# Performance work log

Measured on AMD Instinct MI355X. Metric: run time of the kernel, lower is better.

The kernel has to match this reference:

```python
import jax, jax.numpy as jnp
import numpy as np

EPS = 1e-7
TOTAL_COUNT = 10000.0
BN_EPS = 1e-5
LEAKY_SLOPE = 0.2


def _gcn(h, src, dst, n):
    # GCNConv with add_self_loops=True, bias=False; h = x @ W already applied.
    # deg counts incoming edges at dst plus the self-loop weight of 1.
    deg = jax.ops.segment_sum(jnp.ones(src.shape[0], h.dtype), dst, num_segments=n) + 1.0
    dinv = jax.lax.rsqrt(deg)
    norm = dinv[src] * dinv[dst]                       # [E]
    agg = jax.ops.segment_sum(h[src] * norm[:, None], dst, num_segments=n)
    # self-loop contribution: norm_ii = dinv_i^2
    return agg + (dinv * dinv)[:, None] * h


def _bn(h, gamma, beta):
    # BatchNorm1d, training-mode batch statistics (biased variance)
    mu = h.mean(axis=0)
    var = h.var(axis=0)
    return gamma * (h - mu) * jax.lax.rsqrt(var + BN_EPS) + beta


def _layer(h, W, gamma, beta, src, dst, n):
    h = _gcn(h @ W, src, dst, n)
    h = _bn(h, gamma, beta)
    # LeakyReLU(0.2); Dropout treated as eval-mode identity
    return jnp.where(h >= 0, h, LEAKY_SLOPE * h)


def setup_inputs() -> dict:
    key = jax.random.key(0)
    ks = jax.random.split(key, 8)
    N, E, F_in, H, F_out = 50000, 800000, 1000, 256, 32
    return {
        "x": jax.random.uniform(ks[0], (N, F_in), jnp.float32),
        "W1": jax.random.normal(ks[1], (F_in, H), jnp.float32) * 0.05,
        "gamma1": jnp.ones((H,), jnp.float32),
        "beta1": jnp.zeros((H,), jnp.float32),
        "W2": jax.random.normal(ks[2], (H, H), jnp.float32) * 0.05,
        "gamma2": jnp.ones((H,), jnp.float32),
        "beta2": jnp.zeros((H,), jnp.float32),
        "W_loc": jax.random.normal(ks[3], (H, F_out), jnp.float32) * 0.05,
        "b_loc": jnp.zeros((F_out,), jnp.float32),
        "W_std": jax.random.normal(ks[4], (H, F_out), jnp.float32) * 0.05,
        "b_std": jnp.zeros((F_out,), jnp.float32),
        "edge_index": jax.random.randint(ks[5], (2, E), 0, N),
    }


def reference(x, W1, gamma1, beta1, W2, gamma2, beta2, W_loc, b_loc, W_std, b_std, edge_index):
    n = x.shape[0]
    src, dst = edge_index[0], edge_index[1]
    # normalize='log': library size then log1p of CPM-style scaling
    l = x.sum(axis=1, keepdims=True)                   # [N,1]
    h = jnp.log1p(x * (TOTAL_COUNT / l))
    h = _layer(h, W1, gamma1, beta1, src, dst, n)
    h = _layer(h, W2, gamma2, beta2, src, dst, n)
    loc = h @ W_loc + b_loc
    std = jax.nn.softplus(h @ W_std + b_std) + EPS     # Normal(loc, std) params
    return loc, std, l
```

## Files before the change

kernel.cpp:

```cpp
#include <hip/hip_runtime.h>
#include <hip/hip_bf16.h>


typedef float f32x4 __attribute__((ext_vector_type(4)));
typedef __bf16 bf16x8 __attribute__((ext_vector_type(8)));

#define AS1 __attribute__((address_space(1)))
#define AS3 __attribute__((address_space(3)))

__device__ __forceinline__ void gload_lds16(const void* g, void* l) {
  __builtin_amdgcn_global_load_lds((AS1 void*)(g), (AS3 void*)(l), 16, 0, 0);
}

__device__ __forceinline__ unsigned short f2bu(float f) {
  return __builtin_bit_cast(unsigned short, __float2bfloat16(f));
}
__device__ __forceinline__ float b2f(unsigned short u) {
  return __uint_as_float(((unsigned)u) << 16);
}

__device__ __forceinline__ void unpack8(uint4 v, float* f) {
  f[0] = __uint_as_float(v.x << 16);
  f[1] = __uint_as_float(v.x & 0xffff0000u);
  f[2] = __uint_as_float(v.y << 16);
  f[3] = __uint_as_float(v.y & 0xffff0000u);
  f[4] = __uint_as_float(v.z << 16);
  f[5] = __uint_as_float(v.z & 0xffff0000u);
  f[6] = __uint_as_float(v.w << 16);
  f[7] = __uint_as_float(v.w & 0xffff0000u);
}

__global__ void zero_k(int* __restrict__ p, int n) {
  int i = blockIdx.x * 256 + threadIdx.x;
  if (i < n) p[i] = 0;
}

__global__ void prep_w(const float* __restrict__ W1, const float* __restrict__ W2,
                       const float* __restrict__ Wloc, const float* __restrict__ Wstd,
                       unsigned short* __restrict__ W1T, unsigned short* __restrict__ W2T,
                       unsigned short* __restrict__ WcT) {
  int id = blockIdx.x * 256 + threadIdx.x;
  if (id < 262144) {
    int n = id >> 10, k = id & 1023;
    W1T[n * 1024 + k] = (k < 1000) ? f2bu(W1[k * 256 + n]) : (unsigned short)0;
  } else if (id < 262144 + 65536) {
    int id2 = id - 262144;
    int n = id2 >> 8, k = id2 & 255;
    W2T[n * 256 + k] = f2bu(W2[k * 256 + n]);
  } else if (id < 262144 + 65536 + 16384) {
    int id3 = id - 262144 - 65536;
    int j = id3 >> 8, k = id3 & 255;
    float v = (j < 32) ? Wloc[k * 32 + j] : Wstd[k * 32 + (j - 32)];
    WcT[j * 256 + k] = f2bu(v);
  }
}

__global__ __launch_bounds__(256) void rowsum_k(const float* __restrict__ X,
                                                float* __restrict__ out_l,
                                                unsigned short* __restrict__ xb, int n) {
  int gtid = blockIdx.x * 256 + threadIdx.x;
  int wave = gtid >> 6, lane = gtid & 63;
  int nw = (gridDim.x * 256) >> 6;
  for (int r = wave; r < n; r += nw) {
    const float4* xr = (const float4*)(X + (size_t)r * 1000);
    float4 v0 = xr[lane];
    float4 v1 = xr[lane + 64];
    float4 v2 = xr[lane + 128];
    float4 v3 = (lane < 58) ? xr[lane + 192] : make_float4(0.f, 0.f, 0.f, 0.f);
    float s = ((v0.x + v0.y) + (v0.z + v0.w)) + ((v1.x + v1.y) + (v1.z + v1.w)) +
              ((v2.x + v2.y) + (v2.z + v2.w)) + ((v3.x + v3.y) + (v3.z + v3.w));
#pragma unroll
    for (int o2 = 32; o2 > 0; o2 >>= 1) s += __shfl_xor(s, o2, 64);
    if (lane == 0) out_l[r] = s;
    float sc = 10000.f / s;
    unsigned short* xrow = xb + (size_t)r * 1024;
    ushort4 b;
    b.x = f2bu(__logf(fmaf(v0.x, sc, 1.f)));
    b.y = f2bu(__logf(fmaf(v0.y, sc, 1.f)));
    b.z = f2bu(__logf(fmaf(v0.z, sc, 1.f)));
    b.w = f2bu(__logf(fmaf(v0.w, sc, 1.f)));
    *(ushort4*)(xrow + lane * 4) = b;
    b.x = f2bu(__logf(fmaf(v1.x, sc, 1.f)));
    b.y = f2bu(__logf(fmaf(v1.y, sc, 1.f)));
    b.z = f2bu(__logf(fmaf(v1.z, sc, 1.f)));
    b.w = f2bu(__logf(fmaf(v1.w, sc, 1.f)));
    *(ushort4*)(xrow + (lane + 64) * 4) = b;
    b.x = f2bu(__logf(fmaf(v2.x, sc, 1.f)));
    b.y = f2bu(__logf(fmaf(v2.y, sc, 1.f)));
    b.z = f2bu(__logf(fmaf(v2.z, sc, 1.f)));
    b.w = f2bu(__logf(fmaf(v2.w, sc, 1.f)));
    *(ushort4*)(xrow + (lane + 128) * 4) = b;
    b.x = f2bu(__logf(fmaf(v3.x, sc, 1.f)));
    b.y = f2bu(__logf(fmaf(v3.y, sc, 1.f)));
    b.z = f2bu(__logf(fmaf(v3.z, sc, 1.f)));
    b.w = f2bu(__logf(fmaf(v3.w, sc, 1.f)));
    *(ushort4*)(xrow + (lane + 192) * 4) = b;
  }
}

__global__ void deg_k(const int* __restrict__ ei, int E, int* __restrict__ deg) {
  int e = blockIdx.x * blockDim.x + threadIdx.x;
  int stride = gridDim.x * blockDim.x;
  for (; e < E; e += stride) atomicAdd(&deg[ei[E + e]], 1);
}

__global__ __launch_bounds__(256) void scan1_k(const int* __restrict__ deg, int n,
                                               int* __restrict__ bsum,
                                               float* __restrict__ dinv) {
  int i = blockIdx.x * 256 + threadIdx.x;
  int v = (i < n) ? deg[i] : 0;
  if (i < n) dinv[i] = rsqrtf((float)v + 1.0f);
  __shared__ int sh[256];
  sh[threadIdx.x] = v;
  __syncthreads();
  for (int off = 128; off > 0; off >>= 1) {
    if (threadIdx.x < off) sh[threadIdx.x] += sh[threadIdx.x + off];
    __syncthreads();
  }
  if (threadIdx.x == 0) bsum[blockIdx.x] = sh[0];
}

__global__ __launch_bounds__(256) void scan2_k(int* __restrict__ bsum, int nb) {
  int t = threadIdx.x;
  int v = (t < nb) ? bsum[t] : 0;
  __shared__ int sh[256];
  sh[t] = v;
  __syncthreads();
  for (int off = 1; off < 256; off <<= 1) {
    int u = 0;
    if (t >= off) u = sh[t - off];
    __syncthreads();
    sh[t] += u;
    __syncthreads();
  }
  if (t < nb) bsum[t] = sh[t] - v;
}

__global__ __launch_bounds__(256) void scan3_k(const int* __restrict__ deg, int n, int E,
                                               const int* __restrict__ bsum,
                                               int* __restrict__ row_start,
                                               int* __restrict__ cursor) {
  int i = blockIdx.x * 256 + threadIdx.x;
  int t = threadIdx.x;
  int v = (i < n) ? deg[i] : 0;
  __shared__ int sh[256];
  sh[t] = v;
  __syncthreads();
  for (int off = 1; off < 256; off <<= 1) {
    int u = 0;
    if (t >= off) u = sh[t - off];
    __syncthreads();
    sh[t] += u;
    __syncthreads();
  }
  if (i < n) {
    int rs = bsum[blockIdx.x] + sh[t] - v;
    row_start[i] = rs;
    cursor[i] = rs;
    if (i == n - 1) row_start[n] = E;
  }
}

__global__ void scatter_k(const int* __restrict__ ei, int E,
                          const float* __restrict__ dinv, int* __restrict__ cursor,
                          int2* __restrict__ ew) {
  int e = blockIdx.x * blockDim.x + threadIdx.x;
  int stride = gridDim.x * blockDim.x;
  for (; e < E; e += stride) {
    int s = ei[e], d = ei[E + e];
    float w = dinv[s] * dinv[d];
    int pos = atomicAdd(&cursor[d], 1);
    ew[pos] = make_int2(s, __float_as_int(w));
  }
}

__global__ __launch_bounds__(256) void agg_k(const unsigned short* __restrict__ hg,
                                             const float* __restrict__ dinv,
                                             const int* __restrict__ row_start,
                                             const int2* __restrict__ ew,
                                             unsigned short* __restrict__ hout,
                                             float* __restrict__ psum,
                                             float* __restrict__ psum2, int n) {
  const int tid = threadIdx.x, lane = tid & 63, wid = tid >> 6;
  const int half = lane >> 5;
  const int fl = (lane & 31) * 8;
  int gwave = blockIdx.x * 4 + wid;
  int nw = gridDim.x * 4;
  float bs0 = 0.f, bs1 = 0.f, bs2 = 0.f, bs3 = 0.f;
  float bq0 = 0.f, bq1 = 0.f, bq2 = 0.f, bq3 = 0.f;
  for (int i = gwave; i < n; i += nw) {
    float di = dinv[i];
    float acc[8], f[8];
    {
      uint4 v = *(const uint4*)(hg + (size_t)i * 256 + fl);
      float w0 = half ? 0.f : di * di;
      unpack8(v, f);
#pragma unroll
      for (int q = 0; q < 8; ++q) acc[q] = w0 * f[q];
    }
    int e0 = row_start[i], e1 = row_start[i + 1];
    int j = e0;
    for (; j + 4 <= e1; j += 4) {
      int2 eA = ew[j + half];
      int2 eB = ew[j + 2 + half];
      float wA = __int_as_float(eA.y);
      float wB = __int_as_float(eB.y);
      uint4 vA = *(const uint4*)(hg + (size_t)eA.x * 256 + fl);
      uint4 vB = *(const uint4*)(hg + (size_t)eB.x * 256 + fl);
      float fa[8], fb[8];
      unpack8(vA, fa);
      unpack8(vB, fb);
#pragma unroll
      for (int q = 0; q < 8; ++q) acc[q] = fmaf(wA, fa[q], acc[q]);
#pragma unroll
      for (int q = 0; q < 8; ++q) acc[q] = fmaf(wB, fb[q], acc[q]);
    }
    if (j + 2 <= e1) {
      int2 eA = ew[j + half];
      float wA = __int_as_float(eA.y);
      uint4 vA = *(const uint4*)(hg + (size_t)eA.x * 256 + fl);
      unpack8(vA, f);
#pragma unroll
      for (int q = 0; q < 8; ++q) acc[q] = fmaf(wA, f[q], acc[q]);
      j += 2;
    }
    if (j < e1 && !half) {
      int2 eA = ew[j];
      float wA = __int_as_float(eA.y);
      uint4 vA = *(const uint4*)(hg + (size_t)eA.x * 256 + fl);
      unpack8(vA, f);
#pragma unroll
      for (int q = 0; q < 8; ++q) acc[q] = fmaf(wA, f[q], acc[q]);
    }
#pragma unroll
    for (int q = 0; q < 8; ++q) acc[q] += __shfl_xor(acc[q], 32, 64);
    float o0 = half ? acc[4] : acc[0];
    float o1 = half ? acc[5] : acc[1];
    float o2 = half ? acc[6] : acc[2];
    float o3 = half ? acc[7] : acc[3];
    ushort4 ob;
    ob.x = f2bu(o0); ob.y = f2bu(o1); ob.z = f2bu(o2); ob.w = f2bu(o3);
    *(ushort4*)(hout + (size_t)i * 256 + fl + half * 4) = ob;
    bs0 += o0; bq0 = fmaf(o0, o0, bq0);
    bs1 += o1; bq1 = fmaf(o1, o1, bq1);
    bs2 += o2; bq2 = fmaf(o2, o2, bq2);
    bs3 += o3; bq3 = fmaf(o3, o3, bq3);
  }
  __shared__ float ls[2048];
  int fbase = fl + half * 4;
  *(float4*)&ls[wid * 256 + fbase] = (float4){bs0, bs1, bs2, bs3};
  *(float4*)&ls[1024 + wid * 256 + fbase] = (float4){bq0, bq1, bq2, bq3};
  __syncthreads();
  float ss = ls[tid] + ls[256 + tid] + ls[512 + tid] + ls[768 + tid];
  float qq = ls[1024 + tid] + ls[1280 + tid] + ls[1536 + tid] + ls[1792 + tid];
  psum[(size_t)blockIdx.x * 256 + tid] = ss;
  psum2[(size_t)blockIdx.x * 256 + tid] = qq;
}

__global__ __launch_bounds__(256) void bnfinal_k(const float* __restrict__ psum,
                                                 const float* __restrict__ psum2,
                                                 int nb, int n,
                                                 const float* __restrict__ gamma,
                                                 const float* __restrict__ beta,
                                                 float* __restrict__ bnA,
                                                 float* __restrict__ bnB) {
  int f = blockIdx.x;
  int t = threadIdx.x;
  float s = 0.f, s2 = 0.f;
  for (int b = t; b < nb; b += 256) {
    s += psum[(size_t)b * 256 + f];
    s2 += psum2[(size_t)b * 256 + f];
  }
  __shared__ float as[256], as2[256];
  as[t] = s; as2[t] = s2;
  __syncthreads();
  for (int off = 128; off > 0; off >>= 1) {
    if (t < off) { as[t] += as[t + off]; as2[t] += as2[t + off]; }
    __syncthreads();
  }
  if (t == 0) {
    float m = as[0] / n;
    float var = as2[0] / n - m * m;
    float a = gamma[f] * rsqrtf(var + 1e-5f);
    bnA[f] = a;
    bnB[f] = beta[f] - m * a;
  }
}

template <int KSTEPS, int MODE>
__global__ __launch_bounds__(512) void gemm_kernel(
    const unsigned short* __restrict__ Abf, const unsigned short* __restrict__ Hb,
    const float* __restrict__ bnA, const float* __restrict__ bnB,
    const unsigned short* __restrict__ BT,
    unsigned short* __restrict__ C, int nrows) {
  __shared__ __align__(16) unsigned short At[128 * 64];
  __shared__ __align__(16) unsigned short Bt[256 * 64];
  const int tid = threadIdx.x;
  const int lane = tid & 63;
  const int wid = tid >> 6;
  const int wm = wid >> 2, wn = wid & 3;
  const int brow = blockIdx.x * 128;
  constexpr int K = KSTEPS * 64;

  f32x4 acc[4][4];
#pragma unroll
  for (int m = 0; m < 4; ++m)
#pragma unroll
    for (int n = 0; n < 4; ++n) acc[m][n] = (f32x4){0.f, 0.f, 0.f, 0.f};

  const int rloc = tid >> 4;
  const int hc = tid & 15;
  int growA[4];
#pragma unroll
  for (int p = 0; p < 4; ++p) {
    int r = p * 32 + rloc;
    int g = brow + r;
    if (g > nrows - 1) g = nrows - 1;
    growA[p] = g;
  }

  for (int ks = 0; ks < KSTEPS; ++ks) {
    const int k0 = ks * 64;
#pragma unroll
    for (int is = 0; is < 4; ++is) {
      int n0 = is * 64 + wid * 8;
      int nr = n0 + (lane >> 3);
      int csw = (lane & 7) ^ (lane >> 3);
      gload_lds16(BT + (size_t)nr * K + k0 + csw * 8, Bt + n0 * 64);
    }
    if constexpr (MODE == 0) {
#pragma unroll
      for (int is = 0; is < 2; ++is) {
        int r0 = is * 64 + wid * 8;
        int r = r0 + (lane >> 3);
        int g = brow + r;
        if (g > nrows - 1) g = nrows - 1;
        int csw = (lane & 7) ^ (lane >> 3);
        gload_lds16(Abf + (size_t)g * K + k0 + csw * 8, At + r0 * 64);
      }
    } else {
#pragma unroll
      for (int p = 0; p < 4; ++p) {
        int r = p * 32 + rloc;
        int kk = k0 + hc * 4;
        ushort4 v = *(const ushort4*)(Hb + (size_t)growA[p] * 256 + kk);
        float4 a = *(const float4*)(bnA + kk);
        float4 bb = *(const float4*)(bnB + kk);
        float y0 = fmaf(b2f(v.x), a.x, bb.x); y0 = y0 >= 0.f ? y0 : 0.2f * y0;
        float y1 = fmaf(b2f(v.y), a.y, bb.y); y1 = y1 >= 0.f ? y1 : 0.2f * y1;
        float y2 = fmaf(b2f(v.z), a.z, bb.z); y2 = y2 >= 0.f ? y2 : 0.2f * y2;
        float y3 = fmaf(b2f(v.w), a.w, bb.w); y3 = y3 >= 0.f ? y3 : 0.2f * y3;
        ushort4 b;
        b.x = f2bu(y0); b.y = f2bu(y1); b.z = f2bu(y2); b.w = f2bu(y3);
        *(ushort4*)((char*)At + r * 128 + ((hc * 8) ^ ((r & 7) << 4))) = b;
      }
    }
    __syncthreads();
#pragma unroll
    for (int kk2 = 0; kk2 < 2; ++kk2) {
      const int kb = kk2 * 64 + ((lane >> 4) << 4);
      bf16x8 afr[4], bfr[4];
#pragma unroll
      for (int m = 0; m < 4; ++m) {
        int row = wm * 64 + m * 16 + (lane & 15);
        afr[m] = *(const bf16x8*)((const char*)At + row * 128 + (kb ^ ((row & 7) << 4)));
      }
#pragma unroll
      for (int n = 0; n < 4; ++n) {
        int col = wn * 64 + n * 16 + (lane & 15);
        bfr[n] = *(const bf16x8*)((const char*)Bt + col * 128 + (kb ^ ((col & 7) << 4)));
      }
#pragma unroll
      for (int m = 0; m < 4; ++m)
#pragma unroll
        for (int n = 0; n < 4; ++n)
          acc[m][n] = __builtin_amdgcn_mfma_f32_16x16x32_bf16(afr[m], bfr[n], acc[m][n], 0, 0, 0);
    }
    __syncthreads();
  }
  const int cl = lane & 15;
  const int r4 = (lane >> 4) * 4;
#pragma unroll
  for (int m = 0; m < 4; ++m) {
    int row0 = brow + wm * 64 + m * 16 + r4;
#pragma unroll
    for (int n = 0; n < 4; ++n) {
      int col = wn * 64 + n * 16 + cl;
#pragma unroll
      for (int q = 0; q < 4; ++q) {
        int row = row0 + q;
        if (row < nrows) C[(size_t)row * 256 + col] = f2bu(acc[m][n][q]);
      }
    }
  }
}

__global__ __launch_bounds__(256) void head_kernel(
    const unsigned short* __restrict__ Hb, const float* __restrict__ bnA,
    const float* __restrict__ bnB, const unsigned short* __restrict__ BT,
    const float* __restrict__ bloc, const float* __restrict__ bstd,
    float* __restrict__ out, int nrows) {
  __shared__ __align__(16) unsigned short At[128 * 64];
  __shared__ __align__(16) unsigned short Bt[64 * 64];
  const int tid = threadIdx.x, lane = tid & 63, wid = tid >> 6;
  const int wm = wid >> 1, wn = wid & 1;
  const int brow = blockIdx.x * 128;

  f32x4 acc[4][2];
#pragma unroll
  for (int m = 0; m < 4; ++m)
#pragma unroll
    for (int n = 0; n < 2; ++n) acc[m][n] = (f32x4){0.f, 0.f, 0.f, 0.f};

  const int hc = tid & 15;
  for (int ks = 0; ks < 4; ++ks) {
    const int k0 = ks * 64;
#pragma unroll
    for (int is = 0; is < 2; ++is) {
      int n0 = is * 32 + wid * 8;
      int nr = n0 + (lane >> 3);
      int csw = (lane & 7) ^ (lane >> 3);
      gload_lds16(BT + (size_t)nr * 256 + k0 + csw * 8, Bt + n0 * 64);
    }
#pragma unroll
    for (int p = 0; p < 8; ++p) {
      int r = p * 16 + (tid >> 4);
      int g = brow + r;
      if (g > nrows - 1) g = nrows - 1;
      int kk = k0 + hc * 4;
      ushort4 v = *(const ushort4*)(Hb + (size_t)g * 256 + kk);
      float4 a = *(const float4*)(bnA + kk);
      float4 bb = *(const float4*)(bnB + kk);
      float y0 = fmaf(b2f(v.x), a.x, bb.x); y0 = y0 >= 0.f ? y0 : 0.2f * y0;
      float y1 = fmaf(b2f(v.y), a.y, bb.y); y1 = y1 >= 0.f ? y1 : 0.2f * y1;
      float y2 = fmaf(b2f(v.z), a.z, bb.z); y2 = y2 >= 0.f ? y2 : 0.2f * y2;
      float y3 = fmaf(b2f(v.w), a.w, bb.w); y3 = y3 >= 0.f ? y3 : 0.2f * y3;
      ushort4 b;
      b.x = f2bu(y0); b.y = f2bu(y1); b.z = f2bu(y2); b.w = f2bu(y3);
      *(ushort4*)((char*)At + r * 128 + ((hc * 8) ^ ((r & 7) << 4))) = b;
    }
    __syncthreads();
#pragma unroll
    for (int kk2 = 0; kk2 < 2; ++kk2) {
      const int kb = kk2 * 64 + ((lane >> 4) << 4);
      bf16x8 afr[4], bfr[2];
#pragma unroll
      for (int m = 0; m < 4; ++m) {
        int row = wm * 64 + m * 16 + (lane & 15);
        afr[m] = *(const bf16x8*)((const char*)At + row * 128 + (kb ^ ((row & 7) << 4)));
      }
#pragma unroll
      for (int n = 0; n < 2; ++n) {
        int col = wn * 32 + n * 16 + (lane & 15);
        bfr[n] = *(const bf16x8*)((const char*)Bt + col * 128 + (kb ^ ((col & 7) << 4)));
      }
#pragma unroll
      for (int m = 0; m < 4; ++m)
#pragma unroll
        for (int n = 0; n < 2; ++n)
          acc[m][n] = __builtin_amdgcn_mfma_f32_16x16x32_bf16(afr[m], bfr[n], acc[m][n], 0, 0, 0);
    }
    __syncthreads();
  }
  const int cl = lane & 15;
  const int r4 = (lane >> 4) * 4;
  const size_t stdoff = (size_t)nrows * 32;
#pragma unroll
  for (int m = 0; m < 4; ++m) {
    int row0 = brow + wm * 64 + m * 16 + r4;
#pragma unroll
    for (int n = 0; n < 2; ++n) {
      int j = wn * 32 + n * 16 + cl;
#pragma unroll
      for (int q = 0; q < 4; ++q) {
        int row = row0 + q;
        if (row < nrows) {
          float v = acc[m][n][q];
          if (j < 32) {
            out[(size_t)row * 32 + j] = v + bloc[j];
          } else {
            float xx = v + bstd[j - 32];
            float sp = xx > 20.f ? xx : log1pf(__expf(xx));
            out[stdoff + (size_t)row * 32 + (j - 32)] = sp + 1e-7f;
          }
        }
      }
    }
  }
}

extern "C" void kernel_launch(void* const* d_in, const int* in_sizes, int n_in,
                              void* d_out, int out_size, void* d_ws, size_t ws_size,
                              hipStream_t stream) {
  const float* x = (const float*)d_in[0];
  const float* W1 = (const float*)d_in[1];
  const float* gamma1 = (const float*)d_in[2];
  const float* beta1 = (const float*)d_in[3];
  const float* W2 = (const float*)d_in[4];
  const float* gamma2 = (const float*)d_in[5];
  const float* beta2 = (const float*)d_in[6];
  const float* Wloc = (const float*)d_in[7];
  const float* bloc = (const float*)d_in[8];
  const float* Wstd = (const float*)d_in[9];
  const float* bstd = (const float*)d_in[10];
  const int* ei = (const int*)d_in[11];

  const int N = out_size / 65;
  const int E = in_sizes[11] / 2;
  const int AGG_B = 2048;
  const int SB = (N + 255) / 256;

  char* w = (char*)d_ws;
  size_t off = 0;
  auto alloc = [&](size_t b) -> void* {
    void* p = w + off;
    off = (off + b + 255) & ~(size_t)255;
    return p;
  };

  unsigned short* xb = (unsigned short*)alloc(2 * (size_t)N * 1024);
  unsigned short* W1T = (unsigned short*)alloc(2 * 256 * 1024);
  unsigned short* W2T = (unsigned short*)alloc(2 * 256 * 256);
  unsigned short* WcT = (unsigned short*)alloc(2 * 64 * 256);
  int* deg = (int*)alloc(4 * (size_t)N);
  float* dinv = (float*)alloc(4 * (size_t)N);
  int* row_start = (int*)alloc(4 * ((size_t)N + 1));
  int* cursor = (int*)alloc(4 * (size_t)N);
  int2* ew = (int2*)alloc(8 * (size_t)E);
  int* bsum = (int*)alloc(4 * 256);
  unsigned short* hg = (unsigned short*)alloc(2 * (size_t)N * 256);
  unsigned short* hout = (unsigned short*)alloc(2 * (size_t)N * 256);
  float* psum = (float*)alloc(4 * (size_t)AGG_B * 256);
  float* psum2 = (float*)alloc(4 * (size_t)AGG_B * 256);
  float* bnA1 = (float*)alloc(4 * 256);
  float* bnB1 = (float*)alloc(4 * 256);
  float* bnA2 = (float*)alloc(4 * 256);
  float* bnB2 = (float*)alloc(4 * 256);
  (void)ws_size;

  float* out = (float*)d_out;
  float* out_l = out + (size_t)N * 64;

  const int mb = (N + 127) / 128;

  prep_w<<<1344, 256, 0, stream>>>(W1, W2, Wloc, Wstd, W1T, W2T, WcT);
  rowsum_k<<<2048, 256, 0, stream>>>(x, out_l, xb, N);

  zero_k<<<(N + 255) / 256, 256, 0, stream>>>(deg, N);
  deg_k<<<1024, 256, 0, stream>>>(ei, E, deg);
  scan1_k<<<SB, 256, 0, stream>>>(deg, N, bsum, dinv);
  scan2_k<<<1, 256, 0, stream>>>(bsum, SB);
  scan3_k<<<SB, 256, 0, stream>>>(deg, N, E, bsum, row_start, cursor);
  scatter_k<<<1024, 256, 0, stream>>>(ei, E, dinv, cursor, ew);

  gemm_kernel<16, 0><<<mb, 512, 0, stream>>>(xb, nullptr, nullptr, nullptr, W1T, hg, N);
  agg_k<<<AGG_B, 256, 0, stream>>>(hg, dinv, row_start, ew, hout, psum, psum2, N);
  bnfinal_k<<<256, 256, 0, stream>>>(psum, psum2, AGG_B, N, gamma1, beta1, bnA1, bnB1);

  gemm_kernel<4, 2><<<mb, 512, 0, stream>>>(nullptr, hout, bnA1, bnB1, W2T, hg, N);
  agg_k<<<AGG_B, 256, 0, stream>>>(hg, dinv, row_start, ew, hout, psum, psum2, N);
  bnfinal_k<<<256, 256, 0, stream>>>(psum, psum2, AGG_B, N, gamma2, beta2, bnA2, bnB2);

  head_kernel<<<mb, 256, 0, stream>>>(hout, bnA2, bnB2, WcT, bloc, bstd, out, N);
}
```

Baseline: 368.0 us.

## Fuse graph-prep kernels into independent compute launches for overlap

Merges the degree zeroing into the weight-prep kernel, runs the degree atomics in extra blocks of the rowsum/log kernel, and runs the CSR scatter in extra blocks of the first GEMM launch. This removes several small launches and lets the irregular, atomic-heavy graph work overlap with the bandwidth- and compute-heavy dense stages. The risk is that the extra blocks compete for CUs with the GEMM and rowsum work, or get scheduled after them and so overlap little.

```diff
diff --git a/kernel.cpp b/kernel.cpp
--- a/kernel.cpp
+++ b/kernel.cpp
@@ -30,37 +30,43 @@
   f[7] = __uint_as_float(v.w & 0xffff0000u);
 }
 
-__global__ void zero_k(int* __restrict__ p, int n) {
-  int i = blockIdx.x * 256 + threadIdx.x;
-  if (i < n) p[i] = 0;
-}
-
-__global__ void prep_w(const float* __restrict__ W1, const float* __restrict__ W2,
-                       const float* __restrict__ Wloc, const float* __restrict__ Wstd,
-                       unsigned short* __restrict__ W1T, unsigned short* __restrict__ W2T,
-                       unsigned short* __restrict__ WcT) {
+__global__ void prep_zero_k(const float* __restrict__ W1, const float* __restrict__ W2,
+                            const float* __restrict__ Wloc, const float* __restrict__ Wstd,
+                            unsigned short* __restrict__ W1T, unsigned short* __restrict__ W2T,
+                            unsigned short* __restrict__ WcT, int* __restrict__ deg, int n) {
   int id = blockIdx.x * 256 + threadIdx.x;
   if (id < 262144) {
-    int n = id >> 10, k = id & 1023;
-    W1T[n * 1024 + k] = (k < 1000) ? f2bu(W1[k * 256 + n]) : (unsigned short)0;
+    int nn = id >> 10, k = id & 1023;
+    W1T[nn * 1024 + k] = (k < 1000) ? f2bu(W1[k * 256 + nn]) : (unsigned short)0;
   } else if (id < 262144 + 65536) {
     int id2 = id - 262144;
-    int n = id2 >> 8, k = id2 & 255;
-    W2T[n * 256 + k] = f2bu(W2[k * 256 + n]);
+    int nn = id2 >> 8, k = id2 & 255;
+    W2T[nn * 256 + k] = f2bu(W2[k * 256 + nn]);
   } else if (id < 262144 + 65536 + 16384) {
     int id3 = id - 262144 - 65536;
     int j = id3 >> 8, k = id3 & 255;
     float v = (j < 32) ? Wloc[k * 32 + j] : Wstd[k * 32 + (j - 32)];
     WcT[j * 256 + k] = f2bu(v);
-  }
-}
-
-__global__ __launch_bounds__(256) void rowsum_k(const float* __restrict__ X,
-                                                float* __restrict__ out_l,
-                                                unsigned short* __restrict__ xb, int n) {
+  } else {
+    int id4 = id - 344064;
+    if (id4 < n) deg[id4] = 0;
+  }
+}
+
+__global__ __launch_bounds__(256) void rowsum_deg_k(const float* __restrict__ X,
+                                                    float* __restrict__ out_l,
+                                                    unsigned short* __restrict__ xb, int n,
+                                                    const int* __restrict__ ei, int E,
+                                                    int* __restrict__ deg, int RB) {
+  if (blockIdx.x >= RB) {
+    int e = (blockIdx.x - RB) * 256 + threadIdx.x;
+    int stride = (gridDim.x - RB) * 256;
+    for (; e < E; e += stride) atomicAdd(&deg[ei[E + e]], 1);
+    return;
+  }
   int gtid = blockIdx.x * 256 + threadIdx.x;
   int wave = gtid >> 6, lane = gtid & 63;
-  int nw = (gridDim.x * 256) >> 6;
+  int nw = (RB * 256) >> 6;
   for (int r = wave; r < n; r += nw) {
     const float4* xr = (const float4*)(X + (size_t)r * 1000);
     float4 v0 = xr[lane];
@@ -98,12 +104,6 @@
   }
 }
 
-__global__ void deg_k(const int* __restrict__ ei, int E, int* __restrict__ deg) {
-  int e = blockIdx.x * blockDim.x + threadIdx.x;
-  int stride = gridDim.x * blockDim.x;
-  for (; e < E; e += stride) atomicAdd(&deg[ei[E + e]], 1);
-}
-
 __global__ __launch_bounds__(256) void scan1_k(const int* __restrict__ deg, int n,
                                                int* __restrict__ bsum,
                                                float* __restrict__ dinv) {
@@ -158,19 +158,6 @@
     row_start[i] = rs;
     cursor[i] = rs;
     if (i == n - 1) row_start[n] = E;
-  }
-}
-
-__global__ void scatter_k(const int* __restrict__ ei, int E,
-                          const float* __restrict__ dinv, int* __restrict__ cursor,
-                          int2* __restrict__ ew) {
-  int e = blockIdx.x * blockDim.x + threadIdx.x;
-  int stride = gridDim.x * blockDim.x;
-  for (; e < E; e += stride) {
-    int s = ei[e], d = ei[E + e];
-    float w = dinv[s] * dinv[d];
-    int pos = atomicAdd(&cursor[d], 1);
-    ew[pos] = make_int2(s, __float_as_int(w));
   }
 }
 
@@ -292,7 +279,20 @@
     const unsigned short* __restrict__ Abf, const unsigned short* __restrict__ Hb,
     const float* __restrict__ bnA, const float* __restrict__ bnB,
     const unsigned short* __restrict__ BT,
-    unsigned short* __restrict__ C, int nrows) {
+    unsigned short* __restrict__ C, int nrows,
+    const int* __restrict__ eip, int E, const float* __restrict__ dinvp,
+    int* __restrict__ cursorp, int2* __restrict__ ewp, int mbG) {
+  if (MODE == 0 && blockIdx.x >= mbG) {
+    int e = (blockIdx.x - mbG) * 512 + threadIdx.x;
+    int stride = (gridDim.x - mbG) * 512;
+    for (; e < E; e += stride) {
+      int s = eip[e], d = eip[E + e];
+      float w = dinvp[s] * dinvp[d];
+      int pos = atomicAdd(&cursorp[d], 1);
+      ewp[pos] = make_int2(s, __float_as_int(w));
+    }
+    return;
+  }
   __shared__ __align__(16) unsigned short At[128 * 64];
   __shared__ __align__(16) unsigned short Bt[256 * 64];
   const int tid = threadIdx.x;
@@ -543,21 +543,20 @@
 
   const int mb = (N + 127) / 128;
 
-  prep_w<<<1344, 256, 0, stream>>>(W1, W2, Wloc, Wstd, W1T, W2T, WcT);
-  rowsum_k<<<2048, 256, 0, stream>>>(x, out_l, xb, N);
-
-  zero_k<<<(N + 255) / 256, 256, 0, stream>>>(deg, N);
-  deg_k<<<1024, 256, 0, stream>>>(ei, E, deg);
+  prep_zero_k<<<1344 + SB, 256, 0, stream>>>(W1, W2, Wloc, Wstd, W1T, W2T, WcT, deg, N);
+  rowsum_deg_k<<<2048 + 512, 256, 0, stream>>>(x, out_l, xb, N, ei, E, deg, 2048);
+
   scan1_k<<<SB, 256, 0, stream>>>(deg, N, bsum, dinv);
   scan2_k<<<1, 256, 0, stream>>>(bsum, SB);
   scan3_k<<<SB, 256, 0, stream>>>(deg, N, E, bsum, row_start, cursor);
-  scatter_k<<<1024, 256, 0, stream>>>(ei, E, dinv, cursor, ew);
-
-  gemm_kernel<16, 0><<<mb, 512, 0, stream>>>(xb, nullptr, nullptr, nullptr, W1T, hg, N);
+
+  gemm_kernel<16, 0><<<mb + 512, 512, 0, stream>>>(xb, nullptr, nullptr, nullptr, W1T, hg, N,
+                                                   ei, E, dinv, cursor, ew, mb);
   agg_k<<<AGG_B, 256, 0, stream>>>(hg, dinv, row_start, ew, hout, psum, psum2, N);
   bnfinal_k<<<256, 256, 0, stream>>>(psum, psum2, AGG_B, N, gamma1, beta1, bnA1, bnB1);
 
-  gemm_kernel<4, 2><<<mb, 512, 0, stream>>>(nullptr, hout, bnA1, bnB1, W2T, hg, N);
+  gemm_kernel<4, 2><<<mb, 512, 0, stream>>>(nullptr, hout, bnA1, bnB1, W2T, hg, N,
+                                            nullptr, 0, nullptr, nullptr, nullptr, mb);
   agg_k<<<AGG_B, 256, 0, stream>>>(hg, dinv, row_start, ew, hout, psum, psum2, N);
   bnfinal_k<<<256, 256, 0, stream>>>(psum, psum2, AGG_B, N, gamma2, beta2, bnA2, bnB2);
 
```

After: 340.1 us. 1.08x faster.
